# Optimization experiments

Hardware: AMD Instinct MI355X
Metric: run time of the kernel (lower is better)

The kernel has to match this reference:

```python
import jax, jax.numpy as jnp
import numpy as np

N_NODES = 65536
N_GRAPHS = 1024
NODES_PER_G = 64
N_EDGES = 1048576
IN_FEATS = 512
HIDDEN = 1024
H4 = 256
EMB = 512
EPS = 1e-5
SLOPE = 0.01


def setup_inputs() -> dict:
    key = jax.random.key(0)
    ks = jax.random.split(key, 10)
    # within-graph random edges: edge e belongs to graph e // (E/B)
    epg = N_EDGES // N_GRAPHS
    eg = np.arange(N_EDGES) // epg
    rng = np.random.default_rng(0)
    src = rng.integers(0, NODES_PER_G, N_EDGES) + eg * NODES_PER_G
    dst = rng.integers(0, NODES_PER_G, N_EDGES) + eg * NODES_PER_G
    node_gid = np.arange(N_NODES) // NODES_PER_G
    return {
        "node_feats": jax.random.normal(ks[0], (N_NODES, IN_FEATS), jnp.float32),
        "edge_weights": jax.random.uniform(ks[1], (N_EDGES,), jnp.float32),
        "W1": jax.random.normal(ks[2], (IN_FEATS, HIDDEN), jnp.float32) * 0.05,
        "W2": jax.random.normal(ks[3], (HIDDEN, H4), jnp.float32) * 0.05,
        "W_emb": jax.random.normal(ks[4], (IN_FEATS + HIDDEN + H4, EMB), jnp.float32) * 0.02,
        "gn1_alpha": jnp.ones((HIDDEN,), jnp.float32),
        "gn1_gamma": jnp.ones((HIDDEN,), jnp.float32),
        "gn1_beta": jnp.zeros((HIDDEN,), jnp.float32),
        "gn2_alpha": jnp.ones((H4,), jnp.float32),
        "gn2_gamma": jnp.ones((H4,), jnp.float32),
        "gn2_beta": jnp.zeros((H4,), jnp.float32),
        "edge_src": jnp.asarray(src, jnp.int32),
        "edge_dst": jnp.asarray(dst, jnp.int32),
        "node_gid": jnp.asarray(node_gid, jnp.int32),
    }


def _seg_sum(x, ids, num):
    return jax.ops.segment_sum(x, ids, num_segments=num)


def _graph_conv(x, W, src, dst, ew):
    # DGL GraphConv, norm='both', bias=False, with edge_weight (u_mul_e)
    ones = jnp.ones((src.shape[0],), x.dtype)
    deg_out = jnp.clip(_seg_sum(ones, src, N_NODES), 1.0)
    deg_in = jnp.clip(_seg_sum(ones, dst, N_NODES), 1.0)
    h = (x * jax.lax.rsqrt(deg_out)[:, None]) @ W
    msg = h[src] * ew[:, None]
    agg = _seg_sum(msg, dst, N_NODES)
    return agg * jax.lax.rsqrt(deg_in)[:, None]


def _graph_norm(x, gid, counts, alpha, gamma, beta):
    # GraphNorm (Cai et al.): learnable mean-scale alpha, per-graph stats
    mean = _seg_sum(x, gid, N_GRAPHS) / counts[:, None]
    sub = x - alpha * mean[gid]
    var = _seg_sum(sub * sub, gid, N_GRAPHS) / counts[:, None]
    return gamma * sub * jax.lax.rsqrt(var[gid] + EPS) + beta


def _mean_nodes(x, gid, counts):
    return _seg_sum(x, gid, N_GRAPHS) / counts[:, None]


def _leaky(x):
    return jnp.where(x >= 0, x, SLOPE * x)


def reference(node_feats, edge_weights, W1, W2, W_emb,
              gn1_alpha, gn1_gamma, gn1_beta,
              gn2_alpha, gn2_gamma, gn2_beta,
              edge_src, edge_dst, node_gid):
    counts = jnp.clip(_seg_sum(jnp.ones((N_NODES,), node_feats.dtype), node_gid, N_GRAPHS), 1.0)
    r0 = _mean_nodes(node_feats, node_gid, counts)                 # [B, in]
    h1 = _graph_conv(node_feats, W1, edge_src, edge_dst, edge_weights)
    h1 = _leaky(_graph_norm(h1, node_gid, counts, gn1_alpha, gn1_gamma, gn1_beta))
    r1 = _mean_nodes(h1, node_gid, counts)                          # [B, hidden]
    h2 = _graph_conv(h1, W2, edge_src, edge_dst, edge_weights)
    h2 = _leaky(_graph_norm(h2, node_gid, counts, gn2_alpha, gn2_gamma, gn2_beta))
    r2 = _mean_nodes(h2, node_gid, counts)                          # [B, hidden/4]
    emb = jnp.concatenate([r0, r1, r2], axis=1) @ W_emb             # [B, EMB]
    # InstanceNorm1d on [B, E] input: per-row normalization, no affine
    mu = jnp.mean(emb, axis=1, keepdims=True)
    var = jnp.mean((emb - mu) ** 2, axis=1, keepdims=True)
    emb = (emb - mu) * jax.lax.rsqrt(var + EPS)
    return _leaky(emb)
```

## Files before the change

### kernel.cpp

```cpp
#include <hip/hip_runtime.h>
#include <hip/hip_bf16.h>
#include <stdint.h>

#define N_NODES   65536
#define N_GRAPHS  1024
#define N_EDGES   1048576
#define IN_FEATS  512
#define HIDDEN    1024
#define H4        256
#define EMB_DIM   512
#define RDIM      1792
#define EPS_F     1e-5f
#define SLOPE_F   0.01f

typedef __bf16 bf16;
typedef __bf16 bf16x8 __attribute__((ext_vector_type(8)));
typedef float  floatx4 __attribute__((ext_vector_type(4)));

#define GLDS16(gp, lp) __builtin_amdgcn_global_load_lds( \
    (const __attribute__((address_space(1))) void*)(gp), \
    (__attribute__((address_space(3))) void*)(lp), 16, 0, 0)

__global__ __launch_bounds__(256) void k_graph_build(
    const int* __restrict__ src, const int* __restrict__ dst,
    const float* __restrict__ ew,
    bf16* __restrict__ adjb, float* __restrict__ scl_o)
{
    __shared__ float sAdj[4096];
    __shared__ float sDegO[64], sDegI[64];
    int g = blockIdx.x, tid = threadIdx.x;
    for (int i = tid; i < 4096; i += 256) sAdj[i] = 0.f;
    if (tid < 64) { sDegO[tid] = 0.f; sDegI[tid] = 0.f; }
    __syncthreads();
    int e0 = g * 1024;
    #pragma unroll
    for (int i = 0; i < 4; ++i) {
        int e = e0 + i * 256 + tid;
        int s = src[e] & 63, d = dst[e] & 63;
        atomicAdd(&sAdj[(d << 6) | s], ew[e]);
        atomicAdd(&sDegO[s], 1.f);
        atomicAdd(&sDegI[d], 1.f);
    }
    __syncthreads();
    if (tid < 64) scl_o[g * 64 + tid] = rsqrtf(fmaxf(sDegO[tid], 1.f));
    bf16* ag = adjb + ((size_t)g << 12);
    for (int i = tid; i < 4096; i += 256) {
        float si = rsqrtf(fmaxf(sDegI[i >> 6], 1.f));
        ag[i] = (bf16)(sAdj[i] * si);
    }
}

__global__ __launch_bounds__(256) void k_transpose(
    const float* __restrict__ W, bf16* __restrict__ WT, int K, int logN)
{
    int idx = blockIdx.x * 256 + threadIdx.x;
    if (idx >= (K << logN)) return;
    int n = idx & ((1 << logN) - 1);
    int k = idx >> logN;
    WT[(size_t)n * K + k] = (bf16)W[idx];
}

__global__ __launch_bounds__(256) void k_prep_agg1(
    const float* __restrict__ x, const float* __restrict__ so,
    const bf16* __restrict__ adjb,
    bf16* __restrict__ axs1, bf16* __restrict__ Rb)
{
    __shared__ __align__(16) bf16 sOut[64 * 264];
    __shared__ float sSo[64];
    int g = blockIdx.x >> 1, half = blockIdx.x & 1;
    int tid = threadIdx.x, lane = tid & 63, wave = tid >> 6, q = lane >> 4;
    if (tid < 64) sSo[tid] = so[g * 64 + tid];
    const float* xg = x + (size_t)g * 64 * IN_FEATS + half * 256;
    const bf16* ag = adjb + ((size_t)g << 12);

    bf16x8 af[4][2];
    #pragma unroll
    for (int mt = 0; mt < 4; ++mt)
        #pragma unroll
        for (int kk = 0; kk < 2; ++kk)
            af[mt][kk] = *(const bf16x8*)&ag[(mt * 16 + (lane & 15)) * 64 + kk * 32 + q * 8];
    __syncthreads();
    float sov[2][8];
    #pragma unroll
    for (int kk = 0; kk < 2; ++kk)
        #pragma unroll
        for (int j = 0; j < 8; ++j) sov[kk][j] = sSo[kk * 32 + q * 8 + j];

    #pragma unroll
    for (int nt = 0; nt < 4; ++nt) {
        int cl = wave * 64 + nt * 16 + (lane & 15);
        floatx4 acc[4] = {};
        float r0 = 0.f;
        #pragma unroll
        for (int kk = 0; kk < 2; ++kk) {
            bf16x8 bfrag;
            #pragma unroll
            for (int j = 0; j < 8; ++j) {
                float v = xg[(size_t)(kk * 32 + q * 8 + j) * IN_FEATS + cl];
                r0 += v;
                bfrag[j] = (bf16)(v * sov[kk][j]);
            }
            #pragma unroll
            for (int mt = 0; mt < 4; ++mt)
                acc[mt] = __builtin_amdgcn_mfma_f32_16x16x32_bf16(af[mt][kk], bfrag, acc[mt], 0, 0, 0);
        }
        r0 += __shfl_xor(r0, 16);
        r0 += __shfl_xor(r0, 32);
        if (lane < 16) Rb[(size_t)g * RDIM + half * 256 + cl] = (bf16)(r0 * (1.f / 64.f));
        #pragma unroll
        for (int mt = 0; mt < 4; ++mt)
            #pragma unroll
            for (int i = 0; i < 4; ++i)
                sOut[(mt * 16 + q * 4 + i) * 264 + cl] = (bf16)acc[mt][i];
    }
    __syncthreads();
    #pragma unroll
    for (int it = 0; it < 8; ++it) {
        int idx = it * 256 + tid;
        int d = idx >> 5, c8 = idx & 31;
        *(bf16x8*)&axs1[(size_t)(g * 64 + d) * IN_FEATS + half * 256 + c8 * 8] =
            *(const bf16x8*)&sOut[d * 264 + c8 * 8];
    }
}

__device__ __forceinline__ void gemm_mainloop(
    const bf16* __restrict__ A, const bf16* __restrict__ BT, int K,
    int row0, int col0, int lane, int wave, int wm, int wn, int q,
    bf16* sA, bf16* sB, floatx4 (&acc)[4][4])
{
    for (int k0 = 0; k0 < K; k0 += 64) {
        #pragma unroll
        for (int i = 0; i < 4; ++i) {
            int u = (wave * 4 + i) * 64 + lane;
            int r = u >> 3, p = u & 7;
            int c = p ^ (r & 7);
            GLDS16(A  + (size_t)(row0 + r) * K + (k0 + c * 8), &sA[(wave * 4 + i) * 512]);
            GLDS16(BT + (size_t)(col0 + r) * K + (k0 + c * 8), &sB[(wave * 4 + i) * 512]);
        }
        asm volatile("s_waitcnt vmcnt(0)" ::: "memory");
        __syncthreads();
        #pragma unroll
        for (int kk = 0; kk < 64; kk += 32) {
            bf16x8 afr[4], bfr[4];
            #pragma unroll
            for (int mt = 0; mt < 4; ++mt) {
                int r = wm * 64 + mt * 16 + (lane & 15);
                int c = (kk >> 3) + q;
                afr[mt] = *(const bf16x8*)&sA[(r * 8 + (c ^ (r & 7))) * 8];
            }
            #pragma unroll
            for (int nt = 0; nt < 4; ++nt) {
                int r = wn * 64 + nt * 16 + (lane & 15);
                int c = (kk >> 3) + q;
                bfr[nt] = *(const bf16x8*)&sB[(r * 8 + (c ^ (r & 7))) * 8];
            }
            #pragma unroll
            for (int mt = 0; mt < 4; ++mt)
                #pragma unroll
                for (int nt = 0; nt < 4; ++nt)
                    acc[mt][nt] = __builtin_amdgcn_mfma_f32_16x16x32_bf16(
                        afr[mt], bfr[nt], acc[mt][nt], 0, 0, 0);
        }
        __syncthreads();
    }
}

__device__ __forceinline__ void swizzle_block(int cb, int& bx, int& by)
{
    int b = blockIdx.y * gridDim.x + blockIdx.x;
    int xcd = b & 7, t = b >> 3;
    bx = t % cb;
    by = (t / cb) * 8 + xcd;
}

__global__ __launch_bounds__(256) void k_gemm1_f(
    const bf16* __restrict__ A, const bf16* __restrict__ BT,
    const float* __restrict__ alpha, const float* __restrict__ gamma,
    const float* __restrict__ beta,
    const float* __restrict__ so,
    bf16* __restrict__ xs2, bf16* __restrict__ Rb)
{
    __shared__ __align__(16) bf16 sm[128 * 136];
    __shared__ float sSo[128];
    bf16* sA = sm;
    bf16* sB = sm + 8192;
    const int tid = threadIdx.x;
    const int lane = tid & 63, wave = tid >> 6, q = lane >> 4;
    const int wm = wave & 1, wn = wave >> 1;
    int bx, by; swizzle_block(gridDim.x, bx, by);
    const int row0 = by * 128, col0 = bx * 128;

    if (tid < 128) sSo[tid] = so[row0 + tid];

    floatx4 acc[4][4] = {};
    gemm_mainloop(A, BT, IN_FEATS, row0, col0, lane, wave, wm, wn, q, sA, sB, acc);

    const int gw = by * 2 + wm;
    bf16* sOut = sm;
    #pragma unroll
    for (int nt = 0; nt < 4; ++nt) {
        int cl = wn * 64 + nt * 16 + (lane & 15);
        int colg = col0 + cl;
        float lsum = 0.f;
        #pragma unroll
        for (int mt = 0; mt < 4; ++mt)
            #pragma unroll
            for (int i = 0; i < 4; ++i) lsum += acc[mt][nt][i];
        lsum += __shfl_xor(lsum, 16);
        lsum += __shfl_xor(lsum, 32);
        float am = alpha[colg] * (lsum * (1.f / 64.f));
        float gm = gamma[colg], bt = beta[colg];
        float sub[4][4], qv = 0.f;
        #pragma unroll
        for (int mt = 0; mt < 4; ++mt)
            #pragma unroll
            for (int i = 0; i < 4; ++i) {
                float d = acc[mt][nt][i] - am;
                sub[mt][i] = d; qv += d * d;
            }
        qv += __shfl_xor(qv, 16);
        qv += __shfl_xor(qv, 32);
        float rs = rsqrtf(qv * (1.f / 64.f) + EPS_F);
        float rsum = 0.f;
        #pragma unroll
        for (int mt = 0; mt < 4; ++mt)
            #pragma unroll
            for (int i = 0; i < 4; ++i) {
                float o = gm * sub[mt][i] * rs + bt;
                o = (o >= 0.f) ? o : SLOPE_F * o;
                rsum += o;
                int r = wm * 64 + mt * 16 + q * 4 + i;
                sOut[r * 136 + cl] = (bf16)(o * sSo[r]);
            }
        rsum += __shfl_xor(rsum, 16);
        rsum += __shfl_xor(rsum, 32);
        if (lane < 16)
            Rb[(size_t)gw * RDIM + 512 + colg] = (bf16)(rsum * (1.f / 64.f));
    }
    __syncthreads();
    #pragma unroll
    for (int it = 0; it < 8; ++it) {
        int idx = it * 256 + tid;
        int r = idx >> 4, c8 = idx & 15;
        *(bf16x8*)&xs2[(size_t)(row0 + r) * HIDDEN + col0 + c8 * 8] =
            *(const bf16x8*)&sOut[r * 136 + c8 * 8];
    }
}

__global__ __launch_bounds__(256) void k_gemm2_f(
    const bf16* __restrict__ A, const bf16* __restrict__ BT,
    const bf16* __restrict__ adjb,
    const float* __restrict__ alpha, const float* __restrict__ gamma,
    const float* __restrict__ beta,
    bf16* __restrict__ Rb)
{
    __shared__ __align__(16) bf16 sm[128 * 136];
    bf16* sA = sm;
    bf16* sB = sm + 8192;
    const int tid = threadIdx.x;
    const int lane = tid & 63, wave = tid >> 6, q = lane >> 4;
    const int wm = wave & 1, wn = wave >> 1;
    int bx, by; swizzle_block(gridDim.x, bx, by);
    const int row0 = by * 128, col0 = bx * 128;

    floatx4 acc[4][4] = {};
    gemm_mainloop(A, BT, HIDDEN, row0, col0, lane, wave, wm, wn, q, sA, sB, acc);

    bf16* sT = sm;
    #pragma unroll
    for (int nt = 0; nt < 4; ++nt) {
        int cl = wn * 64 + nt * 16 + (lane & 15);
        #pragma unroll
        for (int mt = 0; mt < 4; ++mt)
            #pragma unroll
            for (int i = 0; i < 4; ++i)
                sT[cl * 136 + wm * 64 + mt * 16 + q * 4 + i] = (bf16)acc[mt][nt][i];
    }
    asm volatile("s_waitcnt lgkmcnt(0)" ::: "memory");

    const int gw = by * 2 + wm;
    const bf16* ag = adjb + ((size_t)gw << 12);
    floatx4 a2[4][4] = {};
    #pragma unroll
    for (int kk = 0; kk < 2; ++kk) {
        bf16x8 afr[4], bfr[4];
        #pragma unroll
        for (int mt = 0; mt < 4; ++mt)
            afr[mt] = *(const bf16x8*)&ag[(mt * 16 + (lane & 15)) * 64 + kk * 32 + q * 8];
        #pragma unroll
        for (int nt = 0; nt < 4; ++nt)
            bfr[nt] = *(const bf16x8*)&sT[(wn * 64 + nt * 16 + (lane & 15)) * 136 + wm * 64 + kk * 32 + q * 8];
        #pragma unroll
        for (int mt = 0; mt < 4; ++mt)
            #pragma unroll
            for (int nt = 0; nt < 4; ++nt)
                a2[mt][nt] = __builtin_amdgcn_mfma_f32_16x16x32_bf16(afr[mt], bfr[nt], a2[mt][nt], 0, 0, 0);
    }

    #pragma unroll
    for (int nt = 0; nt < 4; ++nt) {
        int colg = col0 + wn * 64 + nt * 16 + (lane & 15);
        float lsum = 0.f;
        #pragma unroll
        for (int mt = 0; mt < 4; ++mt)
            #pragma unroll
            for (int i = 0; i < 4; ++i) lsum += a2[mt][nt][i];
        lsum += __shfl_xor(lsum, 16);
        lsum += __shfl_xor(lsum, 32);
        float am = alpha[colg] * (lsum * (1.f / 64.f));
        float gm = gamma[colg], bt = beta[colg];
        float sub[4][4], qv = 0.f;
        #pragma unroll
        for (int mt = 0; mt < 4; ++mt)
            #pragma unroll
            for (int i = 0; i < 4; ++i) {
                float d = a2[mt][nt][i] - am;
                sub[mt][i] = d; qv += d * d;
            }
        qv += __shfl_xor(qv, 16);
        qv += __shfl_xor(qv, 32);
        float rs = rsqrtf(qv * (1.f / 64.f) + EPS_F);
        float rsum = 0.f;
        #pragma unroll
        for (int mt = 0; mt < 4; ++mt)
            #pragma unroll
            for (int i = 0; i < 4; ++i) {
                float o = gm * sub[mt][i] * rs + bt;
                rsum += (o >= 0.f) ? o : SLOPE_F * o;
            }
        rsum += __shfl_xor(rsum, 16);
        rsum += __shfl_xor(rsum, 32);
        if (lane < 16)
            Rb[(size_t)gw * RDIM + 1536 + colg] = (bf16)(rsum * (1.f / 64.f));
    }
}

__global__ __launch_bounds__(256) void k_gemm_ro(
    const bf16* __restrict__ A, const bf16* __restrict__ BT,
    float* __restrict__ Cout)
{
    __shared__ __align__(16) bf16 sm[16384];
    bf16* sA = sm;
    bf16* sB = sm + 8192;
    const int tid = threadIdx.x;
    const int lane = tid & 63, wave = tid >> 6, q = lane >> 4;
    const int wm = wave & 1, wn = wave >> 1;
    int bx, by; swizzle_block(gridDim.x, bx, by);
    const int row0 = by * 128, col0 = bx * 128;

    floatx4 acc[4][4] = {};
    gemm_mainloop(A, BT, RDIM, row0, col0, lane, wave, wm, wn, q, sA, sB, acc);

    #pragma unroll
    for (int mt = 0; mt < 4; ++mt)
        #pragma unroll
        for (int nt = 0; nt < 4; ++nt) {
            int col = col0 + wn * 64 + nt * 16 + (lane & 15);
            #pragma unroll
            for (int i = 0; i < 4; ++i) {
                int row = row0 + wm * 64 + mt * 16 + q * 4 + i;
                Cout[(size_t)row * EMB_DIM + col] = acc[mt][nt][i];
            }
        }
}

__global__ __launch_bounds__(256) void k_instnorm(
    const float* __restrict__ emb, float* __restrict__ out)
{
    int row = blockIdx.x, tid = threadIdx.x;
    int lane = tid & 63, wave = tid >> 6;
    __shared__ float sS[4], sQ[4];
    float v0 = emb[(size_t)row * EMB_DIM + tid];
    float v1 = emb[(size_t)row * EMB_DIM + 256 + tid];
    float s = v0 + v1, q = v0 * v0 + v1 * v1;
    #pragma unroll
    for (int off = 32; off; off >>= 1) {
        s += __shfl_down(s, off);
        q += __shfl_down(q, off);
    }
    if (lane == 0) { sS[wave] = s; sQ[wave] = q; }
    __syncthreads();
    float S = sS[0] + sS[1] + sS[2] + sS[3];
    float Q = sQ[0] + sQ[1] + sQ[2] + sQ[3];
    float mu = S * (1.f / 512.f);
    float var = Q * (1.f / 512.f) - mu * mu;
    float rs = rsqrtf(var + EPS_F);
    float o0 = (v0 - mu) * rs; o0 = (o0 >= 0.f) ? o0 : SLOPE_F * o0;
    float o1 = (v1 - mu) * rs; o1 = (o1 >= 0.f) ? o1 : SLOPE_F * o1;
    out[(size_t)row * EMB_DIM + tid]       = o0;
    out[(size_t)row * EMB_DIM + 256 + tid] = o1;
}

extern "C" void kernel_launch(void* const* d_in, const int* in_sizes, int n_in,
                              void* d_out, int out_size, void* d_ws, size_t ws_size,
                              hipStream_t stream) {
    const float* x    = (const float*)d_in[0];
    const float* ew   = (const float*)d_in[1];
    const float* W1   = (const float*)d_in[2];
    const float* W2   = (const float*)d_in[3];
    const float* Wemb = (const float*)d_in[4];
    const float* a1   = (const float*)d_in[5];
    const float* g1   = (const float*)d_in[6];
    const float* b1   = (const float*)d_in[7];
    const float* a2   = (const float*)d_in[8];
    const float* g2   = (const float*)d_in[9];
    const float* b2   = (const float*)d_in[10];
    const int* esrc   = (const int*)d_in[11];
    const int* edst   = (const int*)d_in[12];
    float* out = (float*)d_out;

    char* ws = (char*)d_ws;
    const size_t MB = 1024ull * 1024ull;
    bf16*  adjb   = (bf16*)(ws);
    float* scl_o  = (float*)(ws + 8 * MB);
    bf16*  Rb     = (bf16*)(ws + 9 * MB);
    bf16*  W1T    = (bf16*)(ws + 13 * MB);
    bf16*  W2T    = (bf16*)(ws + 14 * MB);
    bf16*  WembT  = (bf16*)(ws + 15 * MB);
    float* emb    = (float*)(ws + 17 * MB);
    bf16*  axs1   = (bf16*)(ws + 20 * MB);
    bf16*  xs2    = (bf16*)(ws + 84 * MB);

    k_graph_build<<<N_GRAPHS, 256, 0, stream>>>(esrc, edst, ew, adjb, scl_o);
    k_transpose<<<2048, 256, 0, stream>>>(W1, W1T, 512, 10);
    k_transpose<<<1024, 256, 0, stream>>>(W2, W2T, 1024, 8);
    k_transpose<<<3584, 256, 0, stream>>>(Wemb, WembT, 1792, 9);

    k_prep_agg1<<<N_GRAPHS * 2, 256, 0, stream>>>(x, scl_o, adjb, axs1, Rb);

    k_gemm1_f<<<dim3(HIDDEN / 128, N_NODES / 128), 256, 0, stream>>>(
        axs1, W1T, a1, g1, b1, scl_o, xs2, Rb);
    k_gemm2_f<<<dim3(H4 / 128, N_NODES / 128), 256, 0, stream>>>(
        xs2, W2T, adjb, a2, g2, b2, Rb);
    k_gemm_ro<<<dim3(EMB_DIM / 128, N_GRAPHS / 128), 256, 0, stream>>>(
        Rb, WembT, emb);
    k_instnorm<<<N_GRAPHS, 256, 0, stream>>>(emb, out);

    (void)in_sizes; (void)n_in; (void)out_size; (void)ws_size;
}
```

Measured before the change: 494.3 us.

## Double-buffer LDS tiles in GEMM mainloop to overlap loads with MFMA

Result: faster. 470.6 us (-4.8%).

```diff
diff --git a/kernel.cpp b/kernel.cpp
--- a/kernel.cpp
+++ b/kernel.cpp
@@ -123,36 +123,38 @@
     }
 }
 
-__device__ __forceinline__ void gemm_mainloop(
+__device__ __forceinline__ void gemm_mainloop_db(
     const bf16* __restrict__ A, const bf16* __restrict__ BT, int K,
     int row0, int col0, int lane, int wave, int wm, int wn, int q,
-    bf16* sA, bf16* sB, floatx4 (&acc)[4][4])
-{
-    for (int k0 = 0; k0 < K; k0 += 64) {
+    bf16* sm, floatx4 (&acc)[4][4])
+{
+    auto stage = [&](int k0, int buf) {
         #pragma unroll
         for (int i = 0; i < 4; ++i) {
             int u = (wave * 4 + i) * 64 + lane;
-            int r = u >> 3, p = u & 7;
-            int c = p ^ (r & 7);
-            GLDS16(A  + (size_t)(row0 + r) * K + (k0 + c * 8), &sA[(wave * 4 + i) * 512]);
-            GLDS16(BT + (size_t)(col0 + r) * K + (k0 + c * 8), &sB[(wave * 4 + i) * 512]);
+            int r = u >> 3, c = (u & 7) ^ (r & 7);
+            GLDS16(A  + (size_t)(row0 + r) * K + (k0 + c * 8),
+                   sm + buf * 16384 + (wave * 4 + i) * 512);
+            GLDS16(BT + (size_t)(col0 + r) * K + (k0 + c * 8),
+                   sm + buf * 16384 + 8192 + (wave * 4 + i) * 512);
         }
-        asm volatile("s_waitcnt vmcnt(0)" ::: "memory");
-        __syncthreads();
-        #pragma unroll
-        for (int kk = 0; kk < 64; kk += 32) {
+    };
+    auto step = [&](int buf) {
+        const bf16* sA = sm + buf * 16384;
+        const bf16* sB = sA + 8192;
+        #pragma unroll
+        for (int kk = 0; kk < 2; ++kk) {
             bf16x8 afr[4], bfr[4];
+            int cw = kk * 4 + q;
             #pragma unroll
             for (int mt = 0; mt < 4; ++mt) {
                 int r = wm * 64 + mt * 16 + (lane & 15);
-                int c = (kk >> 3) + q;
-                afr[mt] = *(const bf16x8*)&sA[(r * 8 + (c ^ (r & 7))) * 8];
+                afr[mt] = *(const bf16x8*)&sA[(r * 8 + (cw ^ (r & 7))) * 8];
             }
             #pragma unroll
             for (int nt = 0; nt < 4; ++nt) {
                 int r = wn * 64 + nt * 16 + (lane & 15);
-                int c = (kk >> 3) + q;
-                bfr[nt] = *(const bf16x8*)&sB[(r * 8 + (c ^ (r & 7))) * 8];
+                bfr[nt] = *(const bf16x8*)&sB[(r * 8 + (cw ^ (r & 7))) * 8];
             }
             #pragma unroll
             for (int mt = 0; mt < 4; ++mt)
@@ -161,8 +163,21 @@
                     acc[mt][nt] = __builtin_amdgcn_mfma_f32_16x16x32_bf16(
                         afr[mt], bfr[nt], acc[mt][nt], 0, 0, 0);
         }
+    };
+    stage(0, 0);
+    asm volatile("s_waitcnt vmcnt(0)" ::: "memory");
+    __syncthreads();
+    int cur = 0;
+    const int nsteps = K >> 6;
+    #pragma unroll 1
+    for (int t = 0; t < nsteps - 1; ++t) {
+        stage((t + 1) << 6, cur ^ 1);
+        step(cur);
+        asm volatile("s_waitcnt vmcnt(0)" ::: "memory");
         __syncthreads();
-    }
+        cur ^= 1;
+    }
+    step(cur);
 }
 
 __device__ __forceinline__ void swizzle_block(int cb, int& bx, int& by)
@@ -180,10 +195,8 @@
     const float* __restrict__ so,
     bf16* __restrict__ xs2, bf16* __restrict__ Rb)
 {
-    __shared__ __align__(16) bf16 sm[128 * 136];
+    __shared__ __align__(16) bf16 sm[32768];
     __shared__ float sSo[128];
-    bf16* sA = sm;
-    bf16* sB = sm + 8192;
     const int tid = threadIdx.x;
     const int lane = tid & 63, wave = tid >> 6, q = lane >> 4;
     const int wm = wave & 1, wn = wave >> 1;
@@ -193,7 +206,8 @@
     if (tid < 128) sSo[tid] = so[row0 + tid];
 
     floatx4 acc[4][4] = {};
-    gemm_mainloop(A, BT, IN_FEATS, row0, col0, lane, wave, wm, wn, q, sA, sB, acc);
+    gemm_mainloop_db(A, BT, IN_FEATS, row0, col0, lane, wave, wm, wn, q, sm, acc);
+    __syncthreads();
 
     const int gw = by * 2 + wm;
     bf16* sOut = sm;
@@ -254,9 +268,7 @@
     const float* __restrict__ beta,
     bf16* __restrict__ Rb)
 {
-    __shared__ __align__(16) bf16 sm[128 * 136];
-    bf16* sA = sm;
-    bf16* sB = sm + 8192;
+    __shared__ __align__(16) bf16 sm[32768];
     const int tid = threadIdx.x;
     const int lane = tid & 63, wave = tid >> 6, q = lane >> 4;
     const int wm = wave & 1, wn = wave >> 1;
@@ -264,7 +276,8 @@
     const int row0 = by * 128, col0 = bx * 128;
 
     floatx4 acc[4][4] = {};
-    gemm_mainloop(A, BT, HIDDEN, row0, col0, lane, wave, wm, wn, q, sA, sB, acc);
+    gemm_mainloop_db(A, BT, HIDDEN, row0, col0, lane, wave, wm, wn, q, sm, acc);
+    __syncthreads();
 
     bf16* sT = sm;
     #pragma unroll
@@ -339,9 +352,7 @@
     const bf16* __restrict__ A, const bf16* __restrict__ BT,
     float* __restrict__ Cout)
 {
-    __shared__ __align__(16) bf16 sm[16384];
-    bf16* sA = sm;
-    bf16* sB = sm + 8192;
+    __shared__ __align__(16) bf16 sm[32768];
     const int tid = threadIdx.x;
     const int lane = tid & 63, wave = tid >> 6, q = lane >> 4;
     const int wm = wave & 1, wn = wave >> 1;
@@ -349,7 +360,7 @@
     const int row0 = by * 128, col0 = bx * 128;
 
     floatx4 acc[4][4] = {};
-    gemm_mainloop(A, BT, RDIM, row0, col0, lane, wave, wm, wn, q, sA, sB, acc);
+    gemm_mainloop_db(A, BT, RDIM, row0, col0, lane, wave, wm, wn, q, sm, acc);
 
     #pragma unroll
     for (int mt = 0; mt < 4; ++mt)
```
